# Kernel tuning notes

Measured on AMD Instinct MI355X. Metric: run time of the kernel, lower is better.

## Reference

```python
import jax, jax.numpy as jnp
import numpy as np

B_, L_, C_ = 4, 2048, 384
EXPAND, H_, N_ = 2, 12, 64
DI = EXPAND * C_          # 768 d_inner
DH = DI // H_             # 64 head dim
HID = 4 * C_              # 1536 mlp hidden
EPS = 1e-5


def layernorm(x, g, b):
    mu = jnp.mean(x, -1, keepdims=True)
    var = jnp.mean((x - mu) ** 2, -1, keepdims=True)
    return (x - mu) * jax.lax.rsqrt(var + EPS) * g + b


def ssm_dir(x, Win, bin_, dtb, Alog, D, Wout, bout):
    """Multihead (Mamba2-style) selective scan. x:(B,L,C) -> (B,L,C)."""
    B, L, _ = x.shape
    zxbcdt = x @ Win + bin_  # (B,L, 2*DI+2*N+H)
    z = zxbcdt[..., :DI]
    xs = zxbcdt[..., DI:2 * DI].reshape(B, L, H_, DH)
    Bt = zxbcdt[..., 2 * DI:2 * DI + N_]
    Ct = zxbcdt[..., 2 * DI + N_:2 * DI + 2 * N_]
    dt = jax.nn.softplus(zxbcdt[..., 2 * DI + 2 * N_:] + dtb)  # (B,L,H)
    A = -jnp.exp(Alog)  # (H,)

    def step(h, inp):
        x_t, B_t, C_t, dt_t = inp  # (B,H,DH),(B,N),(B,N),(B,H)
        a = jnp.exp(dt_t * A)  # (B,H)
        h = a[..., None, None] * h + (dt_t[..., None] * x_t)[..., None] * B_t[:, None, None, :]
        y = jnp.einsum('bhdn,bn->bhd', h, C_t)
        return h, y

    h0 = jnp.zeros((B, H_, DH, N_), x.dtype)
    xsT = jnp.moveaxis(xs, 1, 0)
    _, ys = jax.lax.scan(step, h0, (xsT, jnp.moveaxis(Bt, 1, 0), jnp.moveaxis(Ct, 1, 0), jnp.moveaxis(dt, 1, 0)))
    y = jnp.moveaxis(ys, 0, 1) + D.reshape(H_, DH) * xs  # (B,L,H,DH)
    y = y.reshape(B, L, DI) * jax.nn.silu(z)
    return y @ Wout + bout


def reference(points, g1, be1, g2, be2,
              Winf, binf, dtbf, Alogf, Df, Woutf, boutf,
              Winb, binb, dtbb, Alogb, Db, Woutb, boutb,
              W1, b1m, bng, bnb, W2, b2m):
    # --- token mixer (Parallel bidirectional SSM), pre-norm residual ---
    shortcut = points
    x = layernorm(points, g1, be1)
    fwd = ssm_dir(x, Winf, binf, dtbf, Alogf, Df, Woutf, boutf)
    bwd = jnp.flip(ssm_dir(jnp.flip(x, -2), Winb, binb, dtbb, Alogb, Db, Woutb, boutb), -2)
    x = fwd + bwd + shortcut
    # --- channel mixer (Conv1d k=1 == dense), BatchNorm in eval mode ---
    shortcut = x
    h = layernorm(x, g2, be2)
    h = h @ W1.T + b1m  # (B,L,HID)
    h = (h * (bng / np.sqrt(1.0 + EPS))) + bnb  # BN eval, running mean 0 var 1
    h = jax.nn.relu(h)
    h = h @ W2.T + b2m
    return h + shortcut


def setup_inputs() -> dict:
    key = jax.random.key(0)
    ks = jax.random.split(key, 32)
    s = 0.02
    PROJ = 2 * DI + 2 * N_ + H_

    def dir_params(i):
        return dict(
            Win=jax.random.normal(ks[i], (C_, PROJ)) * s,
            bin_=jnp.zeros((PROJ,)),
            dtb=jnp.log(jnp.expm1(jax.random.uniform(ks[i + 1], (H_,), minval=0.001, maxval=0.1))),
            Alog=jnp.log(jnp.arange(1, H_ + 1, dtype=jnp.float32)),
            D=jnp.ones((DI,)),
            Wout=jax.random.normal(ks[i + 2], (DI, C_)) * s,
            bout=jnp.zeros((C_,)))

    f, b = dir_params(1), dir_params(4)
    return {
        'points': jax.random.normal(ks[0], (B_, L_, C_)),
        'g1': jnp.ones((C_,)), 'be1': jnp.zeros((C_,)),
        'g2': jnp.ones((C_,)), 'be2': jnp.zeros((C_,)),
        'Winf': f['Win'], 'binf': f['bin_'], 'dtbf': f['dtb'], 'Alogf': f['Alog'], 'Df': f['D'], 'Woutf': f['Wout'], 'boutf': f['bout'],
        'Winb': b['Win'], 'binb': b['bin_'], 'dtbb': b['dtb'], 'Alogb': b['Alog'], 'Db': b['D'], 'Woutb': b['Wout'], 'boutb': b['bout'],
        'W1': jax.random.normal(ks[7], (HID, C_)) * s, 'b1m': jnp.zeros((HID,)),
        'bng': jnp.ones((HID,)), 'bnb': jnp.zeros((HID,)),
        'W2': jax.random.normal(ks[8], (C_, HID)) * s, 'b2m': jnp.zeros((C_,)),
    }
```

## Files before the change

kernel.cpp:

```cpp
#include <hip/hip_runtime.h>
#include <hip/hip_bf16.h>

typedef unsigned short u16;
typedef unsigned int   u32;

#define DEVINL static __device__ __forceinline__

constexpr int Bb   = 4;
constexpr int Ll   = 2048;
constexpr int Cc   = 384;
constexpr int Hh   = 12;
constexpr int Nn   = 64;
constexpr int DHh  = 64;
constexpr int DIi  = 768;
constexpr int PROJ = 2*DIi + 2*Nn + Hh;
constexpr int PROJp= 1792;
constexpr int HIDh = 1536;
constexpr int TOK  = Bb*Ll;

constexpr int NWINP  = PROJp*Cc;
constexpr int NWOUTC = Cc*2*DIi;
constexpr int NW1    = HIDh*Cc;
constexpr int NW2    = Cc*HIDh;

typedef __attribute__((ext_vector_type(8))) short bf16x8;
typedef __attribute__((ext_vector_type(4))) float f32x4;

DEVINL float u2f(u32 u){ union { u32 i; float f; } c; c.i = u << 16; return c.f; }
DEVINL u16 f2u(float f){
  u32 x = __float_as_uint(f);
  x += 0x7fffu + ((x >> 16) & 1u);
  return (u16)(x >> 16);
}
DEVINL void ld8f(const u16* p, float* f){
  uint2 w0 = *reinterpret_cast<const uint2*>(p);
  uint2 w1 = *reinterpret_cast<const uint2*>(p + 4);
  f[0]=u2f(w0.x & 0xffffu); f[1]=u2f(w0.x >> 16);
  f[2]=u2f(w0.y & 0xffffu); f[3]=u2f(w0.y >> 16);
  f[4]=u2f(w1.x & 0xffffu); f[5]=u2f(w1.x >> 16);
  f[6]=u2f(w1.y & 0xffffu); f[7]=u2f(w1.y >> 16);
}
DEVINL bf16x8 lds_ld8(const u16* p){
  union { uint2 q[2]; bf16x8 v; } r;
  r.q[0] = *reinterpret_cast<const uint2*>(p);
  r.q[1] = *reinterpret_cast<const uint2*>(p + 4);
  return r.v;
}
DEVINL float ing(const void* p, size_t i, bool f32){
  return f32 ? ((const float*)p)[i] : u2f(((const u16*)p)[i]);
}
DEVINL float softplusf(float v){
  if (v > 20.f) return v;
  return log1pf(expf(v));
}
DEVINL float sigmoidf(float z){
  if (z >= 0.f) { return 1.f / (1.f + expf(-z)); }
  float e = expf(z);
  return e / (1.f + e);
}

DEVINL void gload16(const u16* g, u16* l){
  __builtin_amdgcn_global_load_lds(
      (const __attribute__((address_space(1))) void*)g,
      (__attribute__((address_space(3))) void*)l, 16, 0, 0);
}

DEVINL int xcd_swz2d(){
  int nwg = gridDim.x * gridDim.y;
  int bid = blockIdx.y * gridDim.x + blockIdx.x;
  int qc = nwg >> 3, rc = nwg & 7;
  int xcd = bid & 7, loc = bid >> 3;
  return (xcd < rc) ? (xcd*(qc+1) + loc) : (rc*(qc+1) + (xcd-rc)*qc + loc);
}
DEVINL void xcd_cyb(int& c, int& yy, int& b){
  int ny = gridDim.y, nz = gridDim.z;
  int nwg = gridDim.x * ny * nz;
  int lid = (blockIdx.z*ny + blockIdx.y)*gridDim.x + blockIdx.x;
  int qc = nwg >> 3, rc = nwg & 7;
  int xcd = lid & 7, loc = lid >> 3;
  int swz = (xcd < rc) ? (xcd*(qc+1) + loc) : (rc*(qc+1) + (xcd-rc)*qc + loc);
  yy = swz % ny;
  int t = swz / ny;
  b = t % nz;
  c = t / nz;
}

__global__ void detect_kernel(const u32* __restrict__ g1w, u32* __restrict__ flag){
  if (threadIdx.x == 0 && blockIdx.x == 0)
    flag[0] = (g1w[0] == 0x3F800000u) ? 1u : 0u;
}

__global__ __launch_bounds__(256) void wtr_kernel(
    const void* __restrict__ s0, const void* __restrict__ s1,
    const void* __restrict__ s2, const void* __restrict__ s3,
    u16* __restrict__ wt, const u32* __restrict__ flg)
{
  __shared__ u16 t[32][33];
  bool f32 = flg[0] != 0;
  int z = blockIdx.z;
  const void* src = (z==0)? s0 : (z==1)? s1 : (z==2)? s2 : s3;
  const int R    = (z<2)? Cc   : DIi;
  const int Csrc = (z<2)? PROJ : Cc;
  const int Np   = (z<2)? PROJp: Cc;
  const int dstr = (z<2)? Cc   : 2*DIi;
  const int doff = (z==3)? DIi : 0;
  u16* dst = wt + ((z==0)? 0 : (z==1)? NWINP : 2*NWINP);
  int tilesx = Np/32, tilesy = R/32;
  int tid = blockIdx.x;
  if (tid >= tilesx*tilesy) return;
  int n0 = (tid % tilesx)*32, k0 = (tid / tilesx)*32;
  int tx = threadIdx.x & 31, ty = threadIdx.x >> 5;
  #pragma unroll
  for (int rr=0; rr<32; rr+=8){
    int k = k0+ty+rr, n = n0+tx;
    float v = (n < Csrc) ? ing(src, (size_t)k*Csrc + n, f32) : 0.f;
    t[ty+rr][tx] = f2u(v);
  }
  __syncthreads();
  #pragma unroll
  for (int rr=0; rr<32; rr+=8){
    int n = n0+ty+rr, k = k0+tx;
    dst[(size_t)n*dstr + doff + k] = t[tx][ty+rr];
  }
}

__global__ __launch_bounds__(256) void wcvt2_kernel(
    const void* __restrict__ p0, const void* __restrict__ p1,
    u16* __restrict__ out, const u32* __restrict__ flg)
{
  bool f32 = flg[0] != 0;
  int i = blockIdx.x*256 + threadIdx.x;
  if (i >= NW1 + NW2) return;
  const void* src = (i < NW1) ? p0 : p1;
  int off = (i < NW1) ? i : i - NW1;
  out[i] = f32 ? f2u(((const float*)src)[off]) : ((const u16*)src)[off];
}

template<int MODE>
__global__ __launch_bounds__(256) void ln_kernel(
    const void* __restrict__ in, const void* __restrict__ g,
    const void* __restrict__ be, u16* __restrict__ out, const u32* __restrict__ flg)
{
  bool f32 = flg[0] != 0;
  int tok  = blockIdx.x*4 + (threadIdx.x >> 6);
  int lane = threadIdx.x & 63;
  size_t base = (size_t)tok * Cc;
  float v[6];
  #pragma unroll
  for (int j=0;j<6;j++){
    size_t idx = base + lane + 64*j;
    v[j] = (MODE == 1) ? ((const float*)in)[idx] : ing(in, idx, f32);
  }
  float s = 0.f;
  #pragma unroll
  for (int j=0;j<6;j++) s += v[j];
  #pragma unroll
  for (int o=32;o;o>>=1) s += __shfl_xor(s, o, 64);
  float mu = s * (1.0f/Cc);
  float q = 0.f;
  #pragma unroll
  for (int j=0;j<6;j++){ float d = v[j]-mu; q = fmaf(d,d,q); }
  #pragma unroll
  for (int o=32;o;o>>=1) q += __shfl_xor(q, o, 64);
  float rs = rsqrtf(q*(1.0f/Cc) + 1e-5f);
  #pragma unroll
  for (int j=0;j<6;j++){
    int c = lane + 64*j;
    out[base + c] = f2u((v[j]-mu)*rs*ing(g, c, f32) + ing(be, c, f32));
  }
}

template<int EPI, int BM, int BN>
__global__ __launch_bounds__(256) void mgemm_kernel(
    const u16* __restrict__ A, const u16* __restrict__ A2, int KA,
    const u16* __restrict__ Bm,
    int M, int N, int K, int lda,
    const void* __restrict__ bias, const void* __restrict__ bng,
    const void* __restrict__ bnb,  const void* __restrict__ resb, size_t res_off,
    const float* resf, u16* __restrict__ outb, float* outf, void* outv,
    const u32* __restrict__ flg)
{
  constexpr int BK = 64;
  constexpr int WR = (BM == 128) ? 2 : 4;
  constexpr int WC = 4 / WR;
  constexpr int RH = BM / WR;
  constexpr int CW = BN / WC;
  constexpr int SM = RH / 16;
  constexpr int SN = CW / 16;

  bool f32 = flg[0] != 0;
  __shared__ u16 As[BM*BK] __attribute__((aligned(16)));
  __shared__ u16 Bs[BN*BK] __attribute__((aligned(16)));
  const int tid  = threadIdx.x;
  const int lane = tid & 63;
  const int w    = tid >> 6;
  const int q    = lane >> 4;
  const int r16  = lane & 15;
  const int wr   = (WC == 1) ? w : (w >> 1);
  const int wc   = (WC == 1) ? 0 : (w & 1);
  const int swz = xcd_swz2d();
  const int m0 = (swz / gridDim.x) * BM, n0 = (swz % gridDim.x) * BN;

  f32x4 acc[SM][SN] = {};

  const int srow = lane >> 3;
  const int sgl  = lane & 7;

  for (int k0 = 0; k0 < K; k0 += BK) {
    const u16* Ab = A; int kc0 = k0;
    if (KA && k0 >= KA){ Ab = A2; kc0 = k0 - KA; }
    #pragma unroll
    for (int j = 0; j < BM/32; j++){
      int r0  = (w*(BM/32) + j)*8;
      int row = r0 + srow;
      int gl  = sgl ^ (row & 7);
      gload16(Ab + (size_t)(m0+row)*lda + kc0 + gl*8, &As[r0*BK]);
    }
    #pragma unroll
    for (int j = 0; j < BN/32; j++){
      int r0  = (w*(BN/32) + j)*8;
      int row = r0 + srow;
      int gl  = sgl ^ (row & 7);
      gload16(Bm + (size_t)(n0+row)*K + k0 + gl*8, &Bs[r0*BK]);
    }
    __syncthreads();
    #pragma unroll
    for (int kk = 0; kk < 2; kk++){
      bf16x8 af[SM], bfr[SN];
      #pragma unroll
      for (int i=0;i<SM;i++){
        int ar = wr*RH + i*16 + r16;
        af[i] = *reinterpret_cast<const bf16x8*>(&As[ar*BK + (((kk*4+q) ^ (ar&7)) << 3)]);
      }
      #pragma unroll
      for (int s=0;s<SN;s++){
        int br = wc*CW + s*16 + r16;
        bfr[s] = *reinterpret_cast<const bf16x8*>(&Bs[br*BK + (((kk*4+q) ^ (br&7)) << 3)]);
      }
      #pragma unroll
      for (int i=0;i<SM;i++)
        #pragma unroll
        for (int s=0;s<SN;s++)
          acc[i][s] = __builtin_amdgcn_mfma_f32_16x16x32_bf16(af[i], bfr[s], acc[i][s], 0,0,0);
    }
    __syncthreads();
  }

  const float RSQ = 0.9999950000374997f;
  #pragma unroll
  for (int i=0;i<SM;i++){
    #pragma unroll
    for (int s=0;s<SN;s++){
      int gcol = n0 + wc*CW + s*16 + r16;
      if (gcol >= N) continue;
      #pragma unroll
      for (int rr=0;rr<4;rr++){
        int grow = m0 + wr*RH + i*16 + q*4 + rr;
        size_t o = (size_t)grow*N + gcol;
        float v = acc[i][s][rr];
        if constexpr (EPI == 0) {
          outb[o] = f2u(v + ing(bias, gcol, f32));
        } else if constexpr (EPI == 1) {
          outf[o] = v + ing(bias, gcol, f32) + ing(bng, gcol, f32)
                      + ing(resb, res_off + o, f32);
        } else if constexpr (EPI == 2) {
          float t = (v + ing(bias, gcol, f32)) * (ing(bng, gcol, f32) * RSQ) + ing(bnb, gcol, f32);
          outb[o] = f2u(t > 0.f ? t : 0.f);
        } else {
          float t = v + ing(bias, gcol, f32) + resf[o];
          if (f32) ((float*)outv)[o] = t; else ((u16*)outv)[o] = f2u(t);
        }
      }
    }
  }
}


__global__ __launch_bounds__(256) void scan_state_kernel(
    const u16* __restrict__ zx, const void* __restrict__ dtb,
    const void* __restrict__ Alog, u16* __restrict__ states,
    float* __restrict__ P, int dir, int QQ, const u32* __restrict__ flg)
{
  bool f32 = flg[0] != 0;
  int c, h, b;
  xcd_cyb(c, h, b);
  int NC = gridDim.x;
  int lane = threadIdx.x & 63;
  int d0   = (threadIdx.x >> 6) * 16;
  float hst[16];
  #pragma unroll
  for (int j=0;j<16;j++) hst[j] = 0.f;
  float Af = -expf(ing(Alog, h, f32));
  float dtbh = ing(dtb, h, f32);
  float p = 1.f;
  for (int i=0;i<QQ;i++){
    int tl = c*QQ + i;
    int t  = dir ? (Ll-1-tl) : tl;
    size_t row = ((size_t)b*Ll + t) * PROJ;
    float dt = softplusf(u2f(zx[row + 2*DIi + 2*Nn + h]) + dtbh);
    float a  = expf(fmaxf(dt*Af, -80.f));
    float u  = dt * u2f(zx[row + 2*DIi + lane]);
    const u16* xrow = zx + row + DIi + h*DHh + d0;
    #pragma unroll
    for (int j=0;j<16;j++) hst[j] = a*hst[j] + u*u2f(xrow[j]);
    p *= a;
  }
  int g = (b*Hh + h)*NC + c;
  u16* sp = states + (size_t)g*4096;
  #pragma unroll
  for (int j=0;j<16;j++) sp[(d0+j)*64 + lane] = f2u(hst[j]);
  if (threadIdx.x == 0) P[g] = p;
}

__global__ __launch_bounds__(256) void scan_state32m4_kernel(
    const u16* __restrict__ zx, const void* __restrict__ dtb,
    const void* __restrict__ Alog, u16* __restrict__ states,
    float* __restrict__ P, int dir, const u32* __restrict__ flg)
{
  constexpr int Q = 32;
  __shared__ u16 Braw[Q][68];
  __shared__ u16 XT[4][64][36];
  __shared__ u16 BwT[4][64][36];
  __shared__ float wv4[4][Q];
  bool f32 = flg[0] != 0;
  int c, hg, b;
  xcd_cyb(c, hg, b);
  int NC = gridDim.x;
  int tid = threadIdx.x;
  int w = tid >> 6, lane = tid & 63;
  int h = hg*4 + w;
  int q = lane >> 4, r16 = lane & 15;
  int g = (b*Hh + h)*NC + c;
  float Af = -expf(ing(Alog, h, f32));
  float dtbh = ing(dtb, h, f32);

  {
    int i = tid >> 3, p = tid & 7;
    int tl = c*Q + i;
    int t  = dir ? (Ll-1-tl) : tl;
    const u16* sb = zx + ((size_t)b*Ll + t)*PROJ + 2*DIi + p*8;
    uint2 b0 = *reinterpret_cast<const uint2*>(sb);
    uint2 b1 = *reinterpret_cast<const uint2*>(sb + 4);
    *reinterpret_cast<uint2*>(&Braw[i][p*8])   = b0;
    *reinterpret_cast<uint2*>(&Braw[i][p*8+4]) = b1;
  }
  #pragma unroll
  for (int rep=0; rep<4; rep++){
    int j = rep*64 + lane;
    int i = j >> 3, p = j & 7;
    int tl = c*Q + i;
    int t  = dir ? (Ll-1-tl) : tl;
    const u16* sx = zx + ((size_t)b*Ll + t)*PROJ + DIi + h*DHh + p*8;
    uint2 a0 = *reinterpret_cast<const uint2*>(sx);
    uint2 a1 = *reinterpret_cast<const uint2*>(sx + 4);
    u16 tmp[8];
    *reinterpret_cast<uint2*>(&tmp[0]) = a0;
    *reinterpret_cast<uint2*>(&tmp[4]) = a1;
    #pragma unroll
    for (int e=0;e<8;e++) XT[w][p*8+e][i] = tmp[e];
  }
  float dt, la;
  {
    int tl = c*Q + (lane & 31);
    int t  = dir ? (Ll-1-tl) : tl;
    float draw = u2f(zx[((size_t)b*Ll + t)*PROJ + 2*DIi + 2*Nn + h]);
    dt = softplusf(draw + dtbh);
    la = fmaxf(dt*Af, -80.f);
  }
  float L = la;
  #pragma unroll
  for (int off=1; off<32; off<<=1){
    float tv = __shfl_up(L, off, 32);
    if ((lane & 31) >= off) L += tv;
  }
  float Lt = __shfl(L, 31, 32);
  if (lane < Q) wv4[w][lane] = expf(fmaxf(Lt - L, -80.f)) * dt;
  if (lane == 0) P[g] = expf(fmaxf(Lt, -87.f));
  __syncthreads();
  #pragma unroll
  for (int rep=0; rep<4; rep++){
    int j = rep*64 + lane;
    int i = j >> 3, p = j & 7;
    float wsc = wv4[w][i];
    u16 tmp[8];
    *reinterpret_cast<uint2*>(&tmp[0]) = *reinterpret_cast<const uint2*>(&Braw[i][p*8]);
    *reinterpret_cast<uint2*>(&tmp[4]) = *reinterpret_cast<const uint2*>(&Braw[i][p*8+4]);
    #pragma unroll
    for (int e=0;e<8;e++) BwT[w][p*8+e][i] = f2u(wsc * u2f(tmp[e]));
  }
  __syncthreads();

  f32x4 acc[4][4] = {};
  bf16x8 af[4];
  #pragma unroll
  for (int mt=0;mt<4;mt++) af[mt] = lds_ld8(&XT[w][mt*16+r16][q*8]);
  #pragma unroll
  for (int nt=0;nt<4;nt++){
    bf16x8 bf = lds_ld8(&BwT[w][nt*16+r16][q*8]);
    #pragma unroll
    for (int mt=0;mt<4;mt++)
      acc[mt][nt] = __builtin_amdgcn_mfma_f32_16x16x32_bf16(af[mt], bf, acc[mt][nt], 0,0,0);
  }
  u16* sp = states + (size_t)g*4096;
  #pragma unroll
  for (int mt=0;mt<4;mt++)
    #pragma unroll
    for (int nt=0;nt<4;nt++)
      #pragma unroll
      for (int rr=0;rr<4;rr++){
        int d = mt*16 + q*4 + rr, n = nt*16 + r16;
        sp[d*64 + n] = f2u(acc[mt][nt][rr]);
      }
}

template<int NC>
__global__ __launch_bounds__(256) void scan_combine_kernel(
    u16* __restrict__ states, const float* __restrict__ P)
{
  __shared__ float ps[(NC > 64) ? NC : 64];
  int g   = blockIdx.x >> 4;
  int idx = ((blockIdx.x & 15) << 8) | threadIdx.x;
  if (threadIdx.x < NC) ps[threadIdx.x] = P[g*NC + threadIdx.x];
  __syncthreads();
  size_t base = (size_t)g*NC*4096 + idx;
  float sv[NC];
  #pragma unroll
  for (int c=0;c<NC;c++) sv[c] = u2f(states[base + (size_t)c*4096]);
  float hr = 0.f;
  #pragma unroll
  for (int c=0;c<NC;c++){
    states[base + (size_t)c*4096] = f2u(hr);
    hr = ps[c]*hr + sv[c];
  }
}

__global__ __launch_bounds__(64) void scan_out_kernel(
    const u16* __restrict__ zx, const void* __restrict__ dtb,
    const void* __restrict__ Alog, const void* __restrict__ Dp,
    const u16* __restrict__ hinit, u16* __restrict__ ych, int dir, int QQ,
    const u32* __restrict__ flg)
{
  bool f32 = flg[0] != 0;
  int c, h, b;
  xcd_cyb(c, h, b);
  int NC = gridDim.x;
  int lane = threadIdx.x;
  int g = (b*Hh + h)*NC + c;
  float hs[64];
  const u16* hp = hinit + (size_t)g*4096 + lane*64;
  #pragma unroll
  for (int n=0;n<64;n++) hs[n] = u2f(hp[n]);
  float Af = -expf(ing(Alog, h, f32));
  float dtbh = ing(dtb, h, f32);
  float Dv = ing(Dp, h*DHh + lane, f32);
  for (int i=0;i<QQ;i++){
    int tl = c*QQ + i;
    int t  = dir ? (Ll-1-tl) : tl;
    size_t row = ((size_t)b*Ll + t) * PROJ;
    float dt = softplusf(u2f(zx[row + 2*DIi + 2*Nn + h]) + dtbh);
    float a  = expf(fmaxf(dt*Af, -80.f));
    float xv = u2f(zx[row + DIi + h*DHh + lane]);
    float zv = u2f(zx[row + h*DHh + lane]);
    const u16* Brow = zx + row + 2*DIi;
    const u16* Crow = Brow + Nn;
    float u = dt * xv;
    float y0=0.f, y1=0.f, y2=0.f, y3=0.f;
    #pragma unroll
    for (int j=0;j<16;j++){
      float h0 = a*hs[j]    + u*u2f(Brow[j]);    hs[j]   =h0; y0 = fmaf(h0, u2f(Crow[j]),    y0);
      float h1 = a*hs[j+16] + u*u2f(Brow[j+16]); hs[j+16]=h1; y1 = fmaf(h1, u2f(Crow[j+16]), y1);
      float h2 = a*hs[j+32] + u*u2f(Brow[j+32]); hs[j+32]=h2; y2 = fmaf(h2, u2f(Crow[j+32]), y2);
      float h3 = a*hs[j+48] + u*u2f(Brow[j+48]); hs[j+48]=h3; y3 = fmaf(h3, u2f(Crow[j+48]), y3);
    }
    float y = (y0+y1)+(y2+y3);
    float yo = y + Dv*xv;
    float sg = zv * sigmoidf(zv);
    ych[((size_t)(b*Ll + t))*DIi + h*DHh + lane] = f2u(yo * sg);
  }
}

__global__ __launch_bounds__(256) void scan_out32m4_kernel(
    const u16* __restrict__ zx, const void* __restrict__ dtb,
    const void* __restrict__ Alog, const void* __restrict__ Dp,
    const u16* __restrict__ hinit, u16* __restrict__ ych, int dir,
    const u32* __restrict__ flg)
{
  constexpr int Q = 32;
  __shared__ u16 bc[Q][132];
  __shared__ u16 XT[4][64][36];
  __shared__ u16 gp[4][Q][36];
  __shared__ float Lss[4][Q], dts[4][Q];
  bool f32 = flg[0] != 0;
  int c, hg, b;
  xcd_cyb(c, hg, b);
  int NC = gridDim.x;
  int tid = threadIdx.x;
  int w = tid >> 6, lane = tid & 63;
  int h = hg*4 + w;
  int q = lane >> 4, r16 = lane & 15;
  int g = (b*Hh + h)*NC + c;
  float Af = -expf(ing(Alog, h, f32));
  float dtbh = ing(dtb, h, f32);

  #pragma unroll
  for (int rep=0; rep<2; rep++){
    int j = rep*256 + tid;
    int i = j >> 4, p = j & 15;
    int tl = c*Q + i;
    int t  = dir ? (Ll-1-tl) : tl;
    const u16* sb = zx + ((size_t)b*Ll + t)*PROJ + 2*DIi + p*8;
    uint2 b0 = *reinterpret_cast<const uint2*>(sb);
    uint2 b1 = *reinterpret_cast<const uint2*>(sb + 4);
    *reinterpret_cast<uint2*>(&bc[i][p*8])   = b0;
    *reinterpret_cast<uint2*>(&bc[i][p*8+4]) = b1;
  }
  #pragma unroll
  for (int rep=0; rep<4; rep++){
    int j = rep*64 + lane;
    int i = j >> 3, p = j & 7;
    int tl = c*Q + i;
    int t  = dir ? (Ll-1-tl) : tl;
    const u16* sx = zx + ((size_t)b*Ll + t)*PROJ + DIi + h*DHh + p*8;
    uint2 a0 = *reinterpret_cast<const uint2*>(sx);
    uint2 a1 = *reinterpret_cast<const uint2*>(sx + 4);
    u16 tmp[8];
    *reinterpret_cast<uint2*>(&tmp[0]) = a0;
    *reinterpret_cast<uint2*>(&tmp[4]) = a1;
    #pragma unroll
    for (int e=0;e<8;e++) XT[w][p*8+e][i] = tmp[e];
  }
  float dt, la;
  {
    int tl = c*Q + (lane & 31);
    int t  = dir ? (Ll-1-tl) : tl;
    float draw = u2f(zx[((size_t)b*Ll + t)*PROJ + 2*DIi + 2*Nn + h]);
    dt = softplusf(draw + dtbh);
    la = fmaxf(dt*Af, -80.f);
  }
  float L = la;
  #pragma unroll
  for (int off=1; off<32; off<<=1){
    float tv = __shfl_up(L, off, 32);
    if ((lane & 31) >= off) L += tv;
  }
  if (lane < Q){ Lss[w][lane] = L; dts[w][lane] = dt; }
  __syncthreads();

  f32x4 gacc[2][2] = {};
  #pragma unroll
  for (int kk=0; kk<2; kk++){
    bf16x8 ac[2], bb[2];
    #pragma unroll
    for (int mt=0;mt<2;mt++) ac[mt] = lds_ld8(&bc[mt*16+r16][64 + kk*32 + q*8]);
    #pragma unroll
    for (int nt=0;nt<2;nt++) bb[nt] = lds_ld8(&bc[nt*16+r16][kk*32 + q*8]);
    #pragma unroll
    for (int mt=0;mt<2;mt++)
      #pragma unroll
      for (int nt=0;nt<2;nt++)
        gacc[mt][nt] = __builtin_amdgcn_mfma_f32_16x16x32_bf16(ac[mt], bb[nt], gacc[mt][nt], 0,0,0);
  }
  float iL[2][4], sL[2], sdt[2];
  #pragma unroll
  for (int mt=0;mt<2;mt++)
    #pragma unroll
    for (int rr=0;rr<4;rr++) iL[mt][rr] = Lss[w][mt*16 + q*4 + rr];
  #pragma unroll
  for (int nt=0;nt<2;nt++){ int s = nt*16 + r16; sL[nt] = Lss[w][s]; sdt[nt] = dts[w][s]; }
  #pragma unroll
  for (int mt=0;mt<2;mt++)
    #pragma unroll
    for (int nt=0;nt<2;nt++)
      #pragma unroll
      for (int rr=0;rr<4;rr++){
        int i = mt*16 + q*4 + rr, s = nt*16 + r16;
        float m = (i >= s) ? expf(fmaxf(iL[mt][rr]-sL[nt], -80.f))*sdt[nt] : 0.f;
        gp[w][i][s] = f2u(gacc[mt][nt][rr] * m);
      }
  __syncthreads();

  f32x4 aI[2][4] = {}, aS[2][4] = {};
  {
    bf16x8 ag[2];
    #pragma unroll
    for (int mt=0;mt<2;mt++) ag[mt] = lds_ld8(&gp[w][mt*16+r16][q*8]);
    #pragma unroll
    for (int nt=0;nt<4;nt++){
      bf16x8 bx = lds_ld8(&XT[w][nt*16+r16][q*8]);
      #pragma unroll
      for (int mt=0;mt<2;mt++)
        aI[mt][nt] = __builtin_amdgcn_mfma_f32_16x16x32_bf16(ag[mt], bx, aI[mt][nt], 0,0,0);
    }
  }
  #pragma unroll
  for (int kk=0; kk<2; kk++){
    bf16x8 ac[2];
    #pragma unroll
    for (int mt=0;mt<2;mt++) ac[mt] = lds_ld8(&bc[mt*16+r16][64 + kk*32 + q*8]);
    #pragma unroll
    for (int nt=0;nt<4;nt++){
      const u16* hp = hinit + (size_t)g*4096 + (nt*16+r16)*64 + kk*32 + q*8;
      bf16x8 bh = *reinterpret_cast<const bf16x8*>(hp);
      #pragma unroll
      for (int mt=0;mt<2;mt++)
        aS[mt][nt] = __builtin_amdgcn_mfma_f32_16x16x32_bf16(ac[mt], bh, aS[mt][nt], 0,0,0);
    }
  }

  float Dv[4];
  #pragma unroll
  for (int nt=0;nt<4;nt++) Dv[nt] = ing(Dp, h*DHh + nt*16 + r16, f32);
  #pragma unroll
  for (int mt=0;mt<2;mt++)
    #pragma unroll
    for (int rr=0;rr<4;rr++){
      int i = mt*16 + q*4 + rr;
      float ei = expf(fmaxf(iL[mt][rr], -87.f));
      int tl = c*Q + i;
      int t  = dir ? (Ll-1-tl) : tl;
      size_t rowz = ((size_t)b*Ll + t)*PROJ + (size_t)h*DHh;
      size_t obase = ((size_t)(b*Ll + t))*DIi + h*DHh;
      #pragma unroll
      for (int nt=0;nt<4;nt++){
        int d = nt*16 + r16;
        float xv = u2f(XT[w][d][i]);
        float zv = u2f(zx[rowz + d]);
        float y  = aI[mt][nt][rr] + ei*aS[mt][nt][rr] + Dv[nt]*xv;
        ych[obase + d] = f2u(y * zv * sigmoidf(zv));
      }
    }
}

extern "C" void kernel_launch(void* const* d_in, const int* in_sizes, int n_in,
                              void* d_out, int out_size, void* d_ws, size_t ws_size,
                              hipStream_t stream)
{
  (void)in_sizes; (void)n_in; (void)out_size;
  const void* points = d_in[0];
  const void* g1   = d_in[1];
  const void* be1  = d_in[2];
  const void* g2   = d_in[3];
  const void* be2  = d_in[4];
  const void* Win[2]  = { d_in[5],  d_in[12] };
  const void* bin[2]  = { d_in[6],  d_in[13] };
  const void* dtb[2]  = { d_in[7],  d_in[14] };
  const void* Alog[2] = { d_in[8],  d_in[15] };
  const void* Dd[2]   = { d_in[9],  d_in[16] };
  const void* Wout[2] = { d_in[10], d_in[17] };
  const void* bout[2] = { d_in[11], d_in[18] };
  const void* W1   = d_in[19];
  const void* b1m  = d_in[20];
  const void* bng  = d_in[21];
  const void* bnb  = d_in[22];
  const void* W2   = d_in[23];
  const void* b2m  = d_in[24];

  auto align256 = [](size_t x){ return (x + 255) & ~(size_t)255; };
  constexpr size_t ZXB  = (size_t)TOK*PROJ*2;
  constexpr size_t YCHB = (size_t)TOK*DIi*2;
  constexpr size_t MLPB = (size_t)TOK*HIDh*2;
  constexpr size_t XB   = (size_t)TOK*Cc*2;
  constexpr size_t X1B  = (size_t)TOK*Cc*4;
  constexpr size_t WTB  = ((size_t)2*NWINP + NWOUTC + NW1 + NW2) * 2;

  auto scan_bytes = [&](int NCc)->size_t {
    size_t STBc = (size_t)Bb*Hh*NCc*4096*2;
    size_t PBc  = align256((size_t)Bb*Hh*NCc*4);
    return ZXB + 2*YCHB + STBc + PBc + 4096;
  };
  auto need_for = [&](int NCc)->size_t {
    size_t scan = scan_bytes(NCc);
    size_t RBc  = scan > MLPB ? scan : MLPB;
    return 256 + align256(XB) + align256(RBc) + align256(X1B) + align256(WTB) + 4096;
  };
  int NCr = 8;
  if (need_for(16) <= ws_size) NCr = 16;
  if (need_for(32) <= ws_size) NCr = 32;
  if (need_for(64) <= ws_size) NCr = 64;
  const int QQr = Ll / NCr;
  const size_t STB = (size_t)Bb*Hh*NCr*4096*2;
  const size_t SCAN = scan_bytes(NCr);
  const size_t RB = SCAN > MLPB ? SCAN : MLPB;

  char* ws = (char*)d_ws;
  size_t off = 0;
  auto alloc = [&](size_t bytes) -> char* {
    char* p = ws + off;
    off += align256(bytes);
    return p;
  };
  u32*   flag = (u32*)  alloc(256);
  u16*   x    = (u16*)  alloc(XB);
  char*  Rbig =         alloc(RB);
  float* x1   = (float*)alloc(X1B);
  u16*   wt   = (u16*)  alloc(WTB);
  u16*   zx     = (u16*)Rbig;
  u16*   ych0   = (u16*)(Rbig + ZXB);
  u16*   ych1   = (u16*)(Rbig + ZXB + YCHB);
  u16*   states = (u16*)(Rbig + ZXB + 2*YCHB);
  float* P      = (float*)(Rbig + ZXB + 2*YCHB + STB);
  u16*   hin2   = x;
  u16*   hmid   = (u16*)Rbig;
  u16* WinT[2]  = { wt, wt + NWINP };
  u16* WoutTT   = wt + 2*NWINP;
  u16* W1b      = wt + 2*NWINP + NWOUTC;
  u16* W2b      = W1b + NW1;
  u16* ychd[2]  = { ych0, ych1 };

  detect_kernel<<<1, 64, 0, stream>>>((const u32*)g1, flag);

  wtr_kernel<<<dim3(672,1,4), 256, 0, stream>>>(
      Win[0], Win[1], Wout[0], Wout[1], wt, flag);
  wcvt2_kernel<<<(NW1+NW2+255)/256, 256, 0, stream>>>(W1, W2, W1b, flag);

  ln_kernel<0><<<TOK/4, 256, 0, stream>>>(points, g1, be1, x, flag);

  for (int dir = 0; dir < 2; dir++) {
    mgemm_kernel<0,128,128><<<dim3(PROJp/128, TOK/128), 256, 0, stream>>>(
        x, nullptr, 0, WinT[dir], TOK, PROJ, Cc, Cc, bin[dir],
        nullptr, nullptr, nullptr, 0, nullptr, zx, nullptr, nullptr, flag);
    if (QQr == 32) {
      scan_state32m4_kernel<<<dim3(NCr, Hh/4, Bb), 256, 0, stream>>>(
          zx, dtb[dir], Alog[dir], states, P, dir, flag);
    } else {
      scan_state_kernel<<<dim3(NCr,Hh,Bb), 256, 0, stream>>>(
          zx, dtb[dir], Alog[dir], states, P, dir, QQr, flag);
    }
    if (NCr == 64)      scan_combine_kernel<64><<<Bb*Hh*16, 256, 0, stream>>>(states, P);
    else if (NCr == 32) scan_combine_kernel<32><<<Bb*Hh*16, 256, 0, stream>>>(states, P);
    else if (NCr == 16) scan_combine_kernel<16><<<Bb*Hh*16, 256, 0, stream>>>(states, P);
    else                scan_combine_kernel< 8><<<Bb*Hh*16, 256, 0, stream>>>(states, P);
    if (QQr == 32) {
      scan_out32m4_kernel<<<dim3(NCr, Hh/4, Bb), 256, 0, stream>>>(
          zx, dtb[dir], Alog[dir], Dd[dir], states, ychd[dir], dir, flag);
    } else {
      scan_out_kernel<<<dim3(NCr,Hh,Bb), 64, 0, stream>>>(
          zx, dtb[dir], Alog[dir], Dd[dir], states, ychd[dir], dir, QQr, flag);
    }
  }

  mgemm_kernel<1,64,64><<<dim3(Cc/64, TOK/64), 256, 0, stream>>>(
      ych0, ych1, DIi, WoutTT, TOK, Cc, 2*DIi, DIi, bout[0],
      bout[1], nullptr, points, 0, nullptr,
      nullptr, x1, nullptr, flag);

  ln_kernel<1><<<TOK/4, 256, 0, stream>>>(x1, g2, be2, hin2, flag);

  mgemm_kernel<2,128,128><<<dim3(HIDh/128, TOK/128), 256, 0, stream>>>(
      hin2, nullptr, 0, W1b, TOK, HIDh, Cc, Cc, b1m,
      bng, bnb, nullptr, 0, nullptr, hmid, nullptr, nullptr, flag);

  mgemm_kernel<3,64,64><<<dim3(Cc/64, TOK/64), 256, 0, stream>>>(
      hmid, nullptr, 0, W2b, TOK, Cc, HIDh, HIDh, b2m,
      nullptr, nullptr, nullptr, 0, x1, nullptr, nullptr, d_out, flag);
}
```

Measured before the change: 373.1 us.

## Batch both scan directions into single launches and fuse weight conversion kernels

The forward and backward SSM directions now run together: one input projection GEMM produces both directions' zxbcdt side by side in a widened row, and the state, combine and output scan kernels each launch once with a doubled grid that decodes direction from the z index. The separate W1/W2 conversion kernel is folded into the weight transpose kernel as an extra z slice. The output and MLP-down GEMMs switch from 64x64 to 128x64 tiles. This cuts kernel launches and fills the GPU better in small scan grids, at the cost of a larger zx/state workspace, which may lower the chosen chunk count when the workspace is limited.

```diff
diff --git a/kernel.cpp b/kernel.cpp
--- a/kernel.cpp
+++ b/kernel.cpp
@@ -15,6 +15,7 @@
 constexpr int DIi  = 768;
 constexpr int PROJ = 2*DIi + 2*Nn + Hh;
 constexpr int PROJp= 1792;
+constexpr int ZROW = 2*PROJp;
 constexpr int HIDh = 1536;
 constexpr int TOK  = Bb*Ll;
 
@@ -31,14 +32,6 @@
   u32 x = __float_as_uint(f);
   x += 0x7fffu + ((x >> 16) & 1u);
   return (u16)(x >> 16);
-}
-DEVINL void ld8f(const u16* p, float* f){
-  uint2 w0 = *reinterpret_cast<const uint2*>(p);
-  uint2 w1 = *reinterpret_cast<const uint2*>(p + 4);
-  f[0]=u2f(w0.x & 0xffffu); f[1]=u2f(w0.x >> 16);
-  f[2]=u2f(w0.y & 0xffffu); f[3]=u2f(w0.y >> 16);
-  f[4]=u2f(w1.x & 0xffffu); f[5]=u2f(w1.x >> 16);
-  f[6]=u2f(w1.y & 0xffffu); f[7]=u2f(w1.y >> 16);
 }
 DEVINL bf16x8 lds_ld8(const u16* p){
   union { uint2 q[2]; bf16x8 v; } r;
@@ -72,7 +65,7 @@
   int xcd = bid & 7, loc = bid >> 3;
   return (xcd < rc) ? (xcd*(qc+1) + loc) : (rc*(qc+1) + (xcd-rc)*qc + loc);
 }
-DEVINL void xcd_cyb(int& c, int& yy, int& b){
+DEVINL void xcd_cyb(int& c, int& yy, int& b8){
   int ny = gridDim.y, nz = gridDim.z;
   int nwg = gridDim.x * ny * nz;
   int lid = (blockIdx.z*ny + blockIdx.y)*gridDim.x + blockIdx.x;
@@ -81,7 +74,7 @@
   int swz = (xcd < rc) ? (xcd*(qc+1) + loc) : (rc*(qc+1) + (xcd-rc)*qc + loc);
   yy = swz % ny;
   int t = swz / ny;
-  b = t % nz;
+  b8 = t % nz;
   c = t / nz;
 }
 
@@ -93,11 +86,21 @@
 __global__ __launch_bounds__(256) void wtr_kernel(
     const void* __restrict__ s0, const void* __restrict__ s1,
     const void* __restrict__ s2, const void* __restrict__ s3,
+    const void* __restrict__ s4, const void* __restrict__ s5,
     u16* __restrict__ wt, const u32* __restrict__ flg)
 {
   __shared__ u16 t[32][33];
   bool f32 = flg[0] != 0;
   int z = blockIdx.z;
+  if (z == 4){
+    u16* dst = wt + 2*NWINP + NWOUTC;
+    for (int i = blockIdx.x*256 + threadIdx.x; i < NW1 + NW2; i += gridDim.x*256){
+      const void* src = (i < NW1) ? s4 : s5;
+      int off = (i < NW1) ? i : i - NW1;
+      dst[i] = f32 ? f2u(((const float*)src)[off]) : ((const u16*)src)[off];
+    }
+    return;
+  }
   const void* src = (z==0)? s0 : (z==1)? s1 : (z==2)? s2 : s3;
   const int R    = (z<2)? Cc   : DIi;
   const int Csrc = (z<2)? PROJ : Cc;
@@ -124,18 +127,6 @@
   }
 }
 
-__global__ __launch_bounds__(256) void wcvt2_kernel(
-    const void* __restrict__ p0, const void* __restrict__ p1,
-    u16* __restrict__ out, const u32* __restrict__ flg)
-{
-  bool f32 = flg[0] != 0;
-  int i = blockIdx.x*256 + threadIdx.x;
-  if (i >= NW1 + NW2) return;
-  const void* src = (i < NW1) ? p0 : p1;
-  int off = (i < NW1) ? i : i - NW1;
-  out[i] = f32 ? f2u(((const float*)src)[off]) : ((const u16*)src)[off];
-}
-
 template<int MODE>
 __global__ __launch_bounds__(256) void ln_kernel(
     const void* __restrict__ in, const void* __restrict__ g,
@@ -260,6 +251,12 @@
         float v = acc[i][s][rr];
         if constexpr (EPI == 0) {
           outb[o] = f2u(v + ing(bias, gcol, f32));
+        } else if constexpr (EPI == 5) {
+          int cc = gcol;
+          const void* bp = bias;
+          if (cc >= PROJp) { cc -= PROJp; bp = bng; }
+          if (cc > PROJ-1) cc = PROJ-1;
+          outb[o] = f2u(v + ing(bp, cc, f32));
         } else if constexpr (EPI == 1) {
           outf[o] = v + ing(bias, gcol, f32) + ing(bng, gcol, f32)
                       + ing(resb, res_off + o, f32);
@@ -277,26 +274,29 @@
 
 
 __global__ __launch_bounds__(256) void scan_state_kernel(
-    const u16* __restrict__ zx, const void* __restrict__ dtb,
-    const void* __restrict__ Alog, u16* __restrict__ states,
-    float* __restrict__ P, int dir, int QQ, const u32* __restrict__ flg)
+    const u16* __restrict__ zx, const void* __restrict__ dtb0,
+    const void* __restrict__ dtb1, const void* __restrict__ Alog0,
+    const void* __restrict__ Alog1, u16* __restrict__ states,
+    float* __restrict__ P, int QQ, const u32* __restrict__ flg)
 {
   bool f32 = flg[0] != 0;
-  int c, h, b;
-  xcd_cyb(c, h, b);
+  int c, h, b8;
+  xcd_cyb(c, h, b8);
+  int dir = b8 >> 2, b = b8 & 3;
+  int zoff = dir * PROJp;
   int NC = gridDim.x;
   int lane = threadIdx.x & 63;
   int d0   = (threadIdx.x >> 6) * 16;
   float hst[16];
   #pragma unroll
   for (int j=0;j<16;j++) hst[j] = 0.f;
-  float Af = -expf(ing(Alog, h, f32));
-  float dtbh = ing(dtb, h, f32);
+  float Af = -expf(ing(dir ? Alog1 : Alog0, h, f32));
+  float dtbh = ing(dir ? dtb1 : dtb0, h, f32);
   float p = 1.f;
   for (int i=0;i<QQ;i++){
     int tl = c*QQ + i;
     int t  = dir ? (Ll-1-tl) : tl;
-    size_t row = ((size_t)b*Ll + t) * PROJ;
+    size_t row = ((size_t)b*Ll + t) * ZROW + zoff;
     float dt = softplusf(u2f(zx[row + 2*DIi + 2*Nn + h]) + dtbh);
     float a  = expf(fmaxf(dt*Af, -80.f));
     float u  = dt * u2f(zx[row + 2*DIi + lane]);
@@ -305,7 +305,7 @@
     for (int j=0;j<16;j++) hst[j] = a*hst[j] + u*u2f(xrow[j]);
     p *= a;
   }
-  int g = (b*Hh + h)*NC + c;
+  int g = ((dir*Bb + b)*Hh + h)*NC + c;
   u16* sp = states + (size_t)g*4096;
   #pragma unroll
   for (int j=0;j<16;j++) sp[(d0+j)*64 + lane] = f2u(hst[j]);
@@ -313,9 +313,10 @@
 }
 
 __global__ __launch_bounds__(256) void scan_state32m4_kernel(
-    const u16* __restrict__ zx, const void* __restrict__ dtb,
-    const void* __restrict__ Alog, u16* __restrict__ states,
-    float* __restrict__ P, int dir, const u32* __restrict__ flg)
+    const u16* __restrict__ zx, const void* __restrict__ dtb0,
+    const void* __restrict__ dtb1, const void* __restrict__ Alog0,
+    const void* __restrict__ Alog1, u16* __restrict__ states,
+    float* __restrict__ P, const u32* __restrict__ flg)
 {
   constexpr int Q = 32;
   __shared__ u16 Braw[Q][68];
@@ -323,22 +324,24 @@
   __shared__ u16 BwT[4][64][36];
   __shared__ float wv4[4][Q];
   bool f32 = flg[0] != 0;
-  int c, hg, b;
-  xcd_cyb(c, hg, b);
+  int c, hg, b8;
+  xcd_cyb(c, hg, b8);
+  int dir = b8 >> 2, b = b8 & 3;
+  int zoff = dir * PROJp;
   int NC = gridDim.x;
   int tid = threadIdx.x;
   int w = tid >> 6, lane = tid & 63;
   int h = hg*4 + w;
   int q = lane >> 4, r16 = lane & 15;
-  int g = (b*Hh + h)*NC + c;
-  float Af = -expf(ing(Alog, h, f32));
-  float dtbh = ing(dtb, h, f32);
+  int g = ((dir*Bb + b)*Hh + h)*NC + c;
+  float Af = -expf(ing(dir ? Alog1 : Alog0, h, f32));
+  float dtbh = ing(dir ? dtb1 : dtb0, h, f32);
 
   {
     int i = tid >> 3, p = tid & 7;
     int tl = c*Q + i;
     int t  = dir ? (Ll-1-tl) : tl;
-    const u16* sb = zx + ((size_t)b*Ll + t)*PROJ + 2*DIi + p*8;
+    const u16* sb = zx + ((size_t)b*Ll + t)*ZROW + zoff + 2*DIi + p*8;
     uint2 b0 = *reinterpret_cast<const uint2*>(sb);
     uint2 b1 = *reinterpret_cast<const uint2*>(sb + 4);
     *reinterpret_cast<uint2*>(&Braw[i][p*8])   = b0;
@@ -350,7 +353,7 @@
     int i = j >> 3, p = j & 7;
     int tl = c*Q + i;
     int t  = dir ? (Ll-1-tl) : tl;
-    const u16* sx = zx + ((size_t)b*Ll + t)*PROJ + DIi + h*DHh + p*8;
+    const u16* sx = zx + ((size_t)b*Ll + t)*ZROW + zoff + DIi + h*DHh + p*8;
     uint2 a0 = *reinterpret_cast<const uint2*>(sx);
     uint2 a1 = *reinterpret_cast<const uint2*>(sx + 4);
     u16 tmp[8];
@@ -363,7 +366,7 @@
   {
     int tl = c*Q + (lane & 31);
     int t  = dir ? (Ll-1-tl) : tl;
-    float draw = u2f(zx[((size_t)b*Ll + t)*PROJ + 2*DIi + 2*Nn + h]);
+    float draw = u2f(zx[((size_t)b*Ll + t)*ZROW + zoff + 2*DIi + 2*Nn + h]);
     dt = softplusf(draw + dtbh);
     la = fmaxf(dt*Af, -80.f);
   }
@@ -435,28 +438,32 @@
 }
 
 __global__ __launch_bounds__(64) void scan_out_kernel(
-    const u16* __restrict__ zx, const void* __restrict__ dtb,
-    const void* __restrict__ Alog, const void* __restrict__ Dp,
-    const u16* __restrict__ hinit, u16* __restrict__ ych, int dir, int QQ,
-    const u32* __restrict__ flg)
+    const u16* __restrict__ zx, const void* __restrict__ dtb0,
+    const void* __restrict__ dtb1, const void* __restrict__ Alog0,
+    const void* __restrict__ Alog1, const void* __restrict__ D0,
+    const void* __restrict__ D1, const u16* __restrict__ hinit,
+    u16* __restrict__ ych0, int QQ, const u32* __restrict__ flg)
 {
   bool f32 = flg[0] != 0;
-  int c, h, b;
-  xcd_cyb(c, h, b);
+  int c, h, b8;
+  xcd_cyb(c, h, b8);
+  int dir = b8 >> 2, b = b8 & 3;
+  int zoff = dir * PROJp;
   int NC = gridDim.x;
   int lane = threadIdx.x;
-  int g = (b*Hh + h)*NC + c;
+  int g = ((dir*Bb + b)*Hh + h)*NC + c;
+  u16* ych = ych0 + (size_t)dir*((size_t)TOK*DIi);
   float hs[64];
   const u16* hp = hinit + (size_t)g*4096 + lane*64;
   #pragma unroll
   for (int n=0;n<64;n++) hs[n] = u2f(hp[n]);
-  float Af = -expf(ing(Alog, h, f32));
-  float dtbh = ing(dtb, h, f32);
-  float Dv = ing(Dp, h*DHh + lane, f32);
+  float Af = -expf(ing(dir ? Alog1 : Alog0, h, f32));
+  float dtbh = ing(dir ? dtb1 : dtb0, h, f32);
+  float Dv = ing(dir ? D1 : D0, h*DHh + lane, f32);
   for (int i=0;i<QQ;i++){
     int tl = c*QQ + i;
     int t  = dir ? (Ll-1-tl) : tl;
-    size_t row = ((size_t)b*Ll + t) * PROJ;
+    size_t row = ((size_t)b*Ll + t) * ZROW + zoff;
     float dt = softplusf(u2f(zx[row + 2*DIi + 2*Nn + h]) + dtbh);
     float a  = expf(fmaxf(dt*Af, -80.f));
     float xv = u2f(zx[row + DIi + h*DHh + lane]);
@@ -480,10 +487,11 @@
 }
 
 __global__ __launch_bounds__(256) void scan_out32m4_kernel(
-    const u16* __restrict__ zx, const void* __restrict__ dtb,
-    const void* __restrict__ Alog, const void* __restrict__ Dp,
-    const u16* __restrict__ hinit, u16* __restrict__ ych, int dir,
-    const u32* __restrict__ flg)
+    const u16* __restrict__ zx, const void* __restrict__ dtb0,
+    const void* __restrict__ dtb1, const void* __restrict__ Alog0,
+    const void* __restrict__ Alog1, const void* __restrict__ D0,
+    const void* __restrict__ D1, const u16* __restrict__ hinit,
+    u16* __restrict__ ych0, const u32* __restrict__ flg)
 {
   constexpr int Q = 32;
   __shared__ u16 bc[Q][132];
@@ -491,16 +499,19 @@
   __shared__ u16 gp[4][Q][36];
   __shared__ float Lss[4][Q], dts[4][Q];
   bool f32 = flg[0] != 0;
-  int c, hg, b;
-  xcd_cyb(c, hg, b);
+  int c, hg, b8;
+  xcd_cyb(c, hg, b8);
+  int dir = b8 >> 2, b = b8 & 3;
+  int zoff = dir * PROJp;
   int NC = gridDim.x;
   int tid = threadIdx.x;
   int w = tid >> 6, lane = tid & 63;
   int h = hg*4 + w;
   int q = lane >> 4, r16 = lane & 15;
-  int g = (b*Hh + h)*NC + c;
-  float Af = -expf(ing(Alog, h, f32));
-  float dtbh = ing(dtb, h, f32);
+  int g = ((dir*Bb + b)*Hh + h)*NC + c;
+  u16* ych = ych0 + (size_t)dir*((size_t)TOK*DIi);
+  float Af = -expf(ing(dir ? Alog1 : Alog0, h, f32));
+  float dtbh = ing(dir ? dtb1 : dtb0, h, f32);
 
   #pragma unroll
   for (int rep=0; rep<2; rep++){
@@ -508,7 +519,7 @@
     int i = j >> 4, p = j & 15;
     int tl = c*Q + i;
     int t  = dir ? (Ll-1-tl) : tl;
-    const u16* sb = zx + ((size_t)b*Ll + t)*PROJ + 2*DIi + p*8;
+    const u16* sb = zx + ((size_t)b*Ll + t)*ZROW + zoff + 2*DIi + p*8;
     uint2 b0 = *reinterpret_cast<const uint2*>(sb);
     uint2 b1 = *reinterpret_cast<const uint2*>(sb + 4);
     *reinterpret_cast<uint2*>(&bc[i][p*8])   = b0;
@@ -520,7 +531,7 @@
     int i = j >> 3, p = j & 7;
     int tl = c*Q + i;
     int t  = dir ? (Ll-1-tl) : tl;
-    const u16* sx = zx + ((size_t)b*Ll + t)*PROJ + DIi + h*DHh + p*8;
+    const u16* sx = zx + ((size_t)b*Ll + t)*ZROW + zoff + DIi + h*DHh + p*8;
     uint2 a0 = *reinterpret_cast<const uint2*>(sx);
     uint2 a1 = *reinterpret_cast<const uint2*>(sx + 4);
     u16 tmp[8];
@@ -533,7 +544,7 @@
   {
     int tl = c*Q + (lane & 31);
     int t  = dir ? (Ll-1-tl) : tl;
-    float draw = u2f(zx[((size_t)b*Ll + t)*PROJ + 2*DIi + 2*Nn + h]);
+    float draw = u2f(zx[((size_t)b*Ll + t)*ZROW + zoff + 2*DIi + 2*Nn + h]);
     dt = softplusf(draw + dtbh);
     la = fmaxf(dt*Af, -80.f);
   }
@@ -609,7 +620,7 @@
 
   float Dv[4];
   #pragma unroll
-  for (int nt=0;nt<4;nt++) Dv[nt] = ing(Dp, h*DHh + nt*16 + r16, f32);
+  for (int nt=0;nt<4;nt++) Dv[nt] = ing(dir ? D1 : D0, h*DHh + nt*16 + r16, f32);
   #pragma unroll
   for (int mt=0;mt<2;mt++)
     #pragma unroll
@@ -618,7 +629,7 @@
       float ei = expf(fmaxf(iL[mt][rr], -87.f));
       int tl = c*Q + i;
       int t  = dir ? (Ll-1-tl) : tl;
-      size_t rowz = ((size_t)b*Ll + t)*PROJ + (size_t)h*DHh;
+      size_t rowz = ((size_t)b*Ll + t)*ZROW + zoff + (size_t)h*DHh;
       size_t obase = ((size_t)(b*Ll + t))*DIi + h*DHh;
       #pragma unroll
       for (int nt=0;nt<4;nt++){
@@ -656,7 +667,7 @@
   const void* b2m  = d_in[24];
 
   auto align256 = [](size_t x){ return (x + 255) & ~(size_t)255; };
-  constexpr size_t ZXB  = (size_t)TOK*PROJ*2;
+  constexpr size_t ZXB  = (size_t)TOK*ZROW*2;
   constexpr size_t YCHB = (size_t)TOK*DIi*2;
   constexpr size_t MLPB = (size_t)TOK*HIDh*2;
   constexpr size_t XB   = (size_t)TOK*Cc*2;
@@ -664,8 +675,8 @@
   constexpr size_t WTB  = ((size_t)2*NWINP + NWOUTC + NW1 + NW2) * 2;
 
   auto scan_bytes = [&](int NCc)->size_t {
-    size_t STBc = (size_t)Bb*Hh*NCc*4096*2;
-    size_t PBc  = align256((size_t)Bb*Hh*NCc*4);
+    size_t STBc = (size_t)2*Bb*Hh*NCc*4096*2;
+    size_t PBc  = align256((size_t)2*Bb*Hh*NCc*4);
     return ZXB + 2*YCHB + STBc + PBc + 4096;
   };
   auto need_for = [&](int NCc)->size_t {
@@ -678,7 +689,7 @@
   if (need_for(32) <= ws_size) NCr = 32;
   if (need_for(64) <= ws_size) NCr = 64;
   const int QQr = Ll / NCr;
-  const size_t STB = (size_t)Bb*Hh*NCr*4096*2;
+  const size_t STB = (size_t)2*Bb*Hh*NCr*4096*2;
   const size_t SCAN = scan_bytes(NCr);
   const size_t RB = SCAN > MLPB ? SCAN : MLPB;
 
@@ -701,45 +712,42 @@
   float* P      = (float*)(Rbig + ZXB + 2*YCHB + STB);
   u16*   hin2   = x;
   u16*   hmid   = (u16*)Rbig;
-  u16* WinT[2]  = { wt, wt + NWINP };
+  u16* WinTT    = wt;
   u16* WoutTT   = wt + 2*NWINP;
   u16* W1b      = wt + 2*NWINP + NWOUTC;
   u16* W2b      = W1b + NW1;
-  u16* ychd[2]  = { ych0, ych1 };
 
   detect_kernel<<<1, 64, 0, stream>>>((const u32*)g1, flag);
 
-  wtr_kernel<<<dim3(672,1,4), 256, 0, stream>>>(
-      Win[0], Win[1], Wout[0], Wout[1], wt, flag);
-  wcvt2_kernel<<<(NW1+NW2+255)/256, 256, 0, stream>>>(W1, W2, W1b, flag);
+  wtr_kernel<<<dim3(672,1,5), 256, 0, stream>>>(
+      Win[0], Win[1], Wout[0], Wout[1], W1, W2, wt, flag);
 
   ln_kernel<0><<<TOK/4, 256, 0, stream>>>(points, g1, be1, x, flag);
 
-  for (int dir = 0; dir < 2; dir++) {
-    mgemm_kernel<0,128,128><<<dim3(PROJp/128, TOK/128), 256, 0, stream>>>(
-        x, nullptr, 0, WinT[dir], TOK, PROJ, Cc, Cc, bin[dir],
-        nullptr, nullptr, nullptr, 0, nullptr, zx, nullptr, nullptr, flag);
-    if (QQr == 32) {
-      scan_state32m4_kernel<<<dim3(NCr, Hh/4, Bb), 256, 0, stream>>>(
-          zx, dtb[dir], Alog[dir], states, P, dir, flag);
-    } else {
-      scan_state_kernel<<<dim3(NCr,Hh,Bb), 256, 0, stream>>>(
-          zx, dtb[dir], Alog[dir], states, P, dir, QQr, flag);
-    }
-    if (NCr == 64)      scan_combine_kernel<64><<<Bb*Hh*16, 256, 0, stream>>>(states, P);
-    else if (NCr == 32) scan_combine_kernel<32><<<Bb*Hh*16, 256, 0, stream>>>(states, P);
-    else if (NCr == 16) scan_combine_kernel<16><<<Bb*Hh*16, 256, 0, stream>>>(states, P);
-    else                scan_combine_kernel< 8><<<Bb*Hh*16, 256, 0, stream>>>(states, P);
-    if (QQr == 32) {
-      scan_out32m4_kernel<<<dim3(NCr, Hh/4, Bb), 256, 0, stream>>>(
-          zx, dtb[dir], Alog[dir], Dd[dir], states, ychd[dir], dir, flag);
-    } else {
-      scan_out_kernel<<<dim3(NCr,Hh,Bb), 64, 0, stream>>>(
-          zx, dtb[dir], Alog[dir], Dd[dir], states, ychd[dir], dir, QQr, flag);
-    }
-  }
-
-  mgemm_kernel<1,64,64><<<dim3(Cc/64, TOK/64), 256, 0, stream>>>(
+  mgemm_kernel<5,128,128><<<dim3(ZROW/128, TOK/128), 256, 0, stream>>>(
+      x, nullptr, 0, WinTT, TOK, ZROW, Cc, Cc, bin[0],
+      bin[1], nullptr, nullptr, 0, nullptr, zx, nullptr, nullptr, flag);
+
+  if (QQr == 32) {
+    scan_state32m4_kernel<<<dim3(NCr, Hh/4, 2*Bb), 256, 0, stream>>>(
+        zx, dtb[0], dtb[1], Alog[0], Alog[1], states, P, flag);
+  } else {
+    scan_state_kernel<<<dim3(NCr, Hh, 2*Bb), 256, 0, stream>>>(
+        zx, dtb[0], dtb[1], Alog[0], Alog[1], states, P, QQr, flag);
+  }
+  if (NCr == 64)      scan_combine_kernel<64><<<2*Bb*Hh*16, 256, 0, stream>>>(states, P);
+  else if (NCr == 32) scan_combine_kernel<32><<<2*Bb*Hh*16, 256, 0, stream>>>(states, P);
+  else if (NCr == 16) scan_combine_kernel<16><<<2*Bb*Hh*16, 256, 0, stream>>>(states, P);
+  else                scan_combine_kernel< 8><<<2*Bb*Hh*16, 256, 0, stream>>>(states, P);
+  if (QQr == 32) {
+    scan_out32m4_kernel<<<dim3(NCr, Hh/4, 2*Bb), 256, 0, stream>>>(
+        zx, dtb[0], dtb[1], Alog[0], Alog[1], Dd[0], Dd[1], states, ych0, flag);
+  } else {
+    scan_out_kernel<<<dim3(NCr, Hh, 2*Bb), 64, 0, stream>>>(
+        zx, dtb[0], dtb[1], Alog[0], Alog[1], Dd[0], Dd[1], states, ych0, QQr, flag);
+  }
+
+  mgemm_kernel<1,128,64><<<dim3(Cc/64, TOK/128), 256, 0, stream>>>(
       ych0, ych1, DIi, WoutTT, TOK, Cc, 2*DIi, DIi, bout[0],
       bout[1], nullptr, points, 0, nullptr,
       nullptr, x1, nullptr, flag);
@@ -750,7 +758,7 @@
       hin2, nullptr, 0, W1b, TOK, HIDh, Cc, Cc, b1m,
       bng, bnb, nullptr, 0, nullptr, hmid, nullptr, nullptr, flag);
 
-  mgemm_kernel<3,64,64><<<dim3(Cc/64, TOK/64), 256, 0, stream>>>(
+  mgemm_kernel<3,128,64><<<dim3(Cc/64, TOK/128), 256, 0, stream>>>(
       hmid, nullptr, 0, W2b, TOK, Cc, HIDh, HIDh, b2m,
       nullptr, nullptr, nullptr, 0, x1, nullptr, nullptr, d_out, flag);
 }
```

Result: faster. 362.4 us (-2.9%).
